# Performance work log

Measured on AMD Instinct MI355X. Metric: run time of the kernel, lower is better.

## Reference

```python
import jax, jax.numpy as jnp
import numpy as np

VOCAB = 50000; EMBED = 300; KDIM = 128; KNUM = 21; KSIZES = (1, 2, 3)
B = 32; QLEN = 32; DLEN = 1024


def _kernel_mus(n):
    mus = [1.0]
    bs = 2.0 / (n - 1)
    mus.append(1.0 - bs / 2)
    for i in range(1, n - 1):
        mus.append(mus[i] - bs)
    return np.asarray(mus, np.float32)


def _kernel_sigmas(n):
    return np.asarray([0.001] + [0.1] * (n - 1), np.float32)


def setup_inputs() -> dict:
    key = jax.random.key(0)
    ks = jax.random.split(key, 12)
    inp = {
        'query_ids': jax.random.randint(ks[0], (B, QLEN), 0, VOCAB),
        'query_masks': jnp.ones((B, QLEN), jnp.float32),
        'doc_ids': jax.random.randint(ks[1], (B, DLEN), 0, VOCAB),
        'doc_masks': jnp.ones((B, DLEN), jnp.float32),
        'emb': jax.random.normal(ks[2], (VOCAB, EMBED), jnp.float32) * 0.02,
    }
    for i, k in enumerate(KSIZES):
        inp[f'conv_w{i+1}'] = jax.random.normal(ks[3 + i], (KDIM, EMBED, k), jnp.float32) / np.sqrt(EMBED * k)
        inp[f'conv_b{i+1}'] = jnp.zeros((KDIM,), jnp.float32)
    feat = KNUM * len(KSIZES) ** 2  # 189
    inp['dense_w'] = jax.random.normal(ks[9], (feat, 1), jnp.float32) * 0.05
    inp['dense_b'] = jnp.zeros((1,), jnp.float32)
    return inp


def _conv_relu(x, w, b):
    # x: [B, L, E], w: [O, E, K] -> [B, L-K+1, O] (VALID conv, matches torch Conv1d no padding)
    y = jax.lax.conv_general_dilated(x, w, (1,), 'VALID', dimension_numbers=('NWC', 'OIW', 'NWC'))
    return jax.nn.relu(y + b)


def _matcher(k_enc, k_mask, v_enc, v_mask, mus, sig):
    kn = k_enc / (jnp.linalg.norm(k_enc, axis=-1, keepdims=True) + 1e-13)
    vn = v_enc / (jnp.linalg.norm(v_enc, axis=-1, keepdims=True) + 1e-13)
    inter = jnp.einsum('bqd,bvd->bqv', kn, vn) * (k_mask[:, :, None] * v_mask[:, None, :])
    # multi-Gaussian soft-histogram over similarity: [B, q, v, KNUM]
    ko = jnp.exp(-((inter[..., None] - mus) ** 2) / (2.0 * sig ** 2))
    kde = jnp.log(jnp.maximum(ko.sum(axis=2), 1e-10)) * 0.01  # [B, q, KNUM]
    return (kde * k_mask[..., None]).sum(axis=1)  # [B, KNUM]


def reference(query_ids, query_masks, doc_ids, doc_masks, emb,
              conv_w1, conv_b1, conv_w2, conv_b2, conv_w3, conv_b3,
              dense_w, dense_b):
    mus = jnp.asarray(_kernel_mus(KNUM))
    sig = jnp.asarray(_kernel_sigmas(KNUM))
    qe = emb[query_ids]  # [B, QLEN, E]
    de = emb[doc_ids]    # [B, DLEN, E]
    cw = [(conv_w1, conv_b1), (conv_w2, conv_b2), (conv_w3, conv_b3)]
    q_encs = [_conv_relu(qe, w, b) for w, b in cw]
    d_encs = [_conv_relu(de, w, b) for w, b in cw]
    logits = jnp.concatenate([
        _matcher(q, query_masks[:, :q.shape[1]], d, doc_masks[:, :d.shape[1]], mus, sig)
        for q in q_encs for d in d_encs], axis=1)  # [B, 189]
    score = (logits @ dense_w + dense_b).squeeze(-1)  # [B]
    return score, logits
```

## Files before the change

kernel.cpp:

```cpp
#include <hip/hip_runtime.h>
#include <hip/hip_bf16.h>
#include <math.h>

#define NB 32
#define QL 32
#define DL 1024
#define EMB 300
#define EMBP 320
#define OD 128
#define KNUM 21
#define VOCAB 50000

typedef short short8 __attribute__((ext_vector_type(8)));
typedef float floatx4 __attribute__((ext_vector_type(4)));

static const size_t WP_OFF  = 0;
static const size_t DPK_OFF = 122880;
static const size_t QPK_OFF = 5365760;
static const size_t QH_OFF  = 5529920;
static const size_t QLO_OFF = 5726528;
static const size_t DH_OFF  = 5923136;
static const size_t DLO_OFF = 12214592;
static const size_t ACC_OFF = 18506048;
static const int ACC_SZ = 9 * NB * QL * KNUM;

#define QPLANE 131072
#define DPLANE 4194304

#define MROWS (NB * DL + NB * QL)
#define MTILES 264
#define CONV_BLOCKS (MTILES * 3)

__device__ __constant__ int WPOFF_C[3] = {0, 40960, 122880};

__device__ __forceinline__ void gl_lds16(const ushort* g, char* l) {
    __builtin_amdgcn_global_load_lds(
        (const __attribute__((address_space(1))) unsigned int*)(g),
        (__attribute__((address_space(3))) unsigned int*)(l), 16, 0, 0);
}

__device__ __forceinline__ ushort bf16_bits(float f) {
    __hip_bfloat16 h = __float2bfloat16(f);
    return *reinterpret_cast<ushort*>(&h);
}

__global__ void prep_w_kernel(const float* __restrict__ w1,
                              const float* __restrict__ w2,
                              const float* __restrict__ w3,
                              ushort* __restrict__ wp) {
    int idx = blockIdx.x * 256 + threadIdx.x;
    if (idx >= 245760) return;
    const float* src;
    int k, rel, base;
    if (idx < 40960)        { k = 1; rel = idx;          src = w1; base = 0; }
    else if (idx < 122880)  { k = 2; rel = idx - 40960;  src = w2; base = 40960; }
    else                    { k = 3; rel = idx - 122880; src = w3; base = 122880; }
    int kd = 320 * k;
    int o = rel / kd;
    int jc = rel - o * kd;
    int j = jc / EMBP;
    int c = jc - j * EMBP;
    float f = (c < EMB) ? src[(o * EMB + c) * k + j] : 0.f;
    wp[base + rel] = bf16_bits(f);
}

__global__ void gather_pack(const float* __restrict__ emb,
                            const int* __restrict__ dids, const int* __restrict__ qids,
                            ushort* __restrict__ dpk, ushort* __restrict__ qpk) {
    int idx = blockIdx.x * 256 + threadIdx.x;
    const int DROWS = NB * DL;
    if (idx >= (DROWS + NB * QL + 2) * 40) return;
    int r = idx / 40;
    int c0 = (idx - r * 40) * 8;
    int rid;
    ushort* dst;
    if (r < DROWS) { rid = dids[r]; dst = dpk + (size_t)r * EMBP; }
    else if (r < DROWS + NB * QL) { rid = qids[r - DROWS]; dst = qpk + (size_t)(r - DROWS) * EMBP; }
    else {
        uint4 zz = {0u, 0u, 0u, 0u};
        *reinterpret_cast<uint4*>(qpk + (size_t)(r - DROWS) * EMBP + c0) = zz;
        return;
    }
    const float* erow = emb + (size_t)rid * EMB;
    ushort v[8];
    if (c0 + 8 <= EMB) {
        float4 f0 = *reinterpret_cast<const float4*>(erow + c0);
        float4 f1 = *reinterpret_cast<const float4*>(erow + c0 + 4);
        float fv[8] = {f0.x, f0.y, f0.z, f0.w, f1.x, f1.y, f1.z, f1.w};
#pragma unroll
        for (int i = 0; i < 8; ++i) v[i] = bf16_bits(fv[i]);
    } else {
#pragma unroll
        for (int i = 0; i < 8; ++i) {
            int c = c0 + i;
            v[i] = bf16_bits((c < EMB) ? erow[c] : 0.f);
        }
    }
    *reinterpret_cast<uint4*>(dst + c0) = *reinterpret_cast<uint4*>(v);
}

__global__ __launch_bounds__(256) void conv_mfma(const ushort* __restrict__ xpk,
                                                 const float* __restrict__ dmask,
                                                 const float* __restrict__ qmask,
                                                 const ushort* __restrict__ wp,
                                                 const float* __restrict__ b1,
                                                 const float* __restrict__ b2,
                                                 const float* __restrict__ b3,
                                                 ushort* __restrict__ dh,
                                                 ushort* __restrict__ dlo,
                                                 ushort* __restrict__ qh,
                                                 ushort* __restrict__ qlo) {
    __shared__ __align__(16) char smem[2][33024];

    const int tid = threadIdx.x;
    const int bid = blockIdx.x;
    const int swz = (bid & 7) * (CONV_BLOCKS / 8) + (bid >> 3);
    const int z = swz % 3;
    const int tile = swz / 3;
    const int l0 = tile * 128;

    const int Kdim = EMBP * (z + 1);
    const int nk = 5 * (z + 1);
    const ushort* wpk = wp + WPOFF_C[z];
    const float* bias = (z == 0) ? b1 : ((z == 1) ? b2 : b3);

    const int wave = tid >> 6;
    const int lane = tid & 63;
    const int l15 = lane & 15;
    const int quad = lane >> 4;
    const int wm = wave >> 1;
    const int wn = wave & 1;

    const int srow = lane >> 3;
    const int scol = (lane & 7) * 8;
    const ushort* a0 = xpk + (size_t)(l0 + wave * 8 + srow) * EMBP + scol;
    const ushort* at = xpk + (size_t)(l0 + 128 + srow) * EMBP + scol;
    const ushort* b0 = wpk + (size_t)(wave * 8 + srow) * Kdim + scol;

    auto stage = [&](int buf, int kk) {
        int jj = (kk >= 10) ? 2 : ((kk >= 5) ? 1 : 0);
        int coff = (kk - jj * 5) * 64;
        int koff = kk * 64;
        char* abuf = smem[buf];
        char* bbuf = smem[buf] + 16640;
#pragma unroll
        for (int p = 0; p < 4; ++p)
            gl_lds16(a0 + p * (32 * EMBP) + coff, abuf + p * 4096 + wave * 1024);
        if (wave == 0 && lane < 16)
            gl_lds16(at + coff, abuf + 16384);
#pragma unroll
        for (int p = 0; p < 4; ++p)
            gl_lds16(b0 + (size_t)p * 32 * Kdim + koff, bbuf + p * 4096 + wave * 1024);
    };

    floatx4 acc[4][4];
#pragma unroll
    for (int i = 0; i < 4; ++i)
#pragma unroll
        for (int j = 0; j < 4; ++j) acc[i][j] = (floatx4)0.f;

    stage(0, 0);
    __syncthreads();

    int jjc = 0, ccc = 0;
    int buf = 0;
    for (int kk = 0; kk < nk; ++kk) {
        if (kk + 1 < nk) stage(buf ^ 1, kk + 1);
        const char* Ab = smem[buf];
        const char* Bb = smem[buf] + 16640;
        short8 af[2][4], bf[2][4];
#pragma unroll
        for (int h = 0; h < 2; ++h)
#pragma unroll
            for (int i = 0; i < 4; ++i) {
                af[h][i] = *reinterpret_cast<const short8*>(
                    Ab + (wm * 64 + i * 16 + l15 + jjc) * 128 + h * 64 + quad * 16);
                bf[h][i] = *reinterpret_cast<const short8*>(
                    Bb + (wn * 64 + i * 16 + l15) * 128 + h * 64 + quad * 16);
            }
#pragma unroll
        for (int h = 0; h < 2; ++h)
#pragma unroll
            for (int i = 0; i < 4; ++i)
#pragma unroll
                for (int j = 0; j < 4; ++j)
                    acc[i][j] = __builtin_amdgcn_mfma_f32_16x16x32_bf16(af[h][i], bf[h][j], acc[i][j], 0, 0, 0);
        ++ccc;
        if (ccc == 5) { ccc = 0; ++jjc; }
        __syncthreads();
        buf ^= 1;
    }

    float (*rowsum)[128] = reinterpret_cast<float(*)[128]>(smem);
    float bv[4];
#pragma unroll
    for (int j = 0; j < 4; ++j) bv[j] = bias[wn * 64 + j * 16 + l15];
#pragma unroll
    for (int i = 0; i < 4; ++i)
#pragma unroll
        for (int r = 0; r < 4; ++r) {
            float p = 0.f;
#pragma unroll
            for (int j = 0; j < 4; ++j) {
                float y = fmaxf(acc[i][j][r] + bv[j], 0.f);
                acc[i][j][r] = y;
                p += y * y;
            }
#pragma unroll
            for (int m = 1; m < 16; m <<= 1) p += __shfl_xor(p, m, 64);
            if (l15 == 0) rowsum[wn][wm * 64 + i * 16 + quad * 4 + r] = p;
        }
    __syncthreads();

#pragma unroll
    for (int i = 0; i < 4; ++i) {
#pragma unroll
        for (int rr = 0; rr < 4; ++rr) {
            int rl = wm * 64 + i * 16 + quad * 4 + rr;
            int r = l0 + rl;
            float tot = rowsum[0][rl] + rowsum[1][rl];
            float mv;
            ushort* hp;
            ushort* lp;
            if (r < NB * DL) {
                int l = r & (DL - 1);
                if (l >= DL - z) continue;
                mv = dmask[r];
                size_t base = (size_t)z * DPLANE + (size_t)r * OD;
                hp = dh + base; lp = dlo + base;
            } else {
                int t = r - NB * DL;
                int l = t & (QL - 1);
                if (l >= QL - z) continue;
                mv = qmask[t];
                size_t base = (size_t)z * QPLANE + (size_t)t * OD;
                hp = qh + base; lp = qlo + base;
            }
            float sc = mv / (sqrtf(tot) + 1e-13f);
            int cb = wn * 64 + l15;
#pragma unroll
            for (int j = 0; j < 4; ++j) {
                float v = acc[i][j][rr] * sc;
                __hip_bfloat16 h = __float2bfloat16(v);
                float hf = __bfloat162float(h);
                hp[cb + j * 16] = *reinterpret_cast<ushort*>(&h);
                __hip_bfloat16 l = __float2bfloat16(v - hf);
                lp[cb + j * 16] = *reinterpret_cast<ushort*>(&l);
            }
        }
    }
}

__global__ __launch_bounds__(256, 4) void matcher_kernel(const ushort* __restrict__ qh_g,
                                                         const ushort* __restrict__ ql_g,
                                                         const ushort* __restrict__ vh_g,
                                                         const ushort* __restrict__ vl_g,
                                                         float* __restrict__ accb) {
    __shared__ __align__(16) float Sm[32 * 132];
    __shared__ float stageb[672];

    const int tid = threadIdx.x;
    const int pp = blockIdx.z;
    const int b = blockIdx.y;
    const int v0 = blockIdx.x * 128;
    const int qi = pp / 3;
    const int di = pp - qi * 3;
    const int Vk = 1024 - di;

    const ushort* qhb = qh_g + (size_t)qi * QPLANE + (size_t)b * (QL * OD);
    const ushort* qlb = ql_g + (size_t)qi * QPLANE + (size_t)b * (QL * OD);
    const ushort* vhb = vh_g + (size_t)di * DPLANE + (size_t)b * (DL * OD) + (size_t)v0 * OD;
    const ushort* vlb = vl_g + (size_t)di * DPLANE + (size_t)b * (DL * OD) + (size_t)v0 * OD;

    const int wave = tid >> 6;
    const int lane = tid & 63;
    const int l15 = lane & 15;
    const int quad = lane >> 4;

    floatx4 acc[2][2];
#pragma unroll
    for (int i = 0; i < 2; ++i)
#pragma unroll
        for (int j = 0; j < 2; ++j) acc[i][j] = (floatx4)0.f;

#pragma unroll
    for (int kw = 0; kw < 4; ++kw) {
        const int ko = kw * 32 + quad * 8;
        short8 qh[2], ql[2], vh[2], vl[2];
#pragma unroll
        for (int i = 0; i < 2; ++i) {
            const int qr = i * 16 + l15;
            const int vr = wave * 32 + i * 16 + l15;
            qh[i] = *reinterpret_cast<const short8*>(qhb + qr * OD + ko);
            ql[i] = *reinterpret_cast<const short8*>(qlb + qr * OD + ko);
            vh[i] = *reinterpret_cast<const short8*>(vhb + (size_t)vr * OD + ko);
            vl[i] = *reinterpret_cast<const short8*>(vlb + (size_t)vr * OD + ko);
        }
#pragma unroll
        for (int i = 0; i < 2; ++i)
#pragma unroll
            for (int j = 0; j < 2; ++j) {
                acc[i][j] = __builtin_amdgcn_mfma_f32_16x16x32_bf16(qh[i], vh[j], acc[i][j], 0, 0, 0);
                acc[i][j] = __builtin_amdgcn_mfma_f32_16x16x32_bf16(qh[i], vl[j], acc[i][j], 0, 0, 0);
                acc[i][j] = __builtin_amdgcn_mfma_f32_16x16x32_bf16(ql[i], vh[j], acc[i][j], 0, 0, 0);
            }
    }

    const int vmax = min(128, Vk - v0);
#pragma unroll
    for (int i = 0; i < 2; ++i)
#pragma unroll
        for (int j = 0; j < 2; ++j)
#pragma unroll
            for (int r = 0; r < 4; ++r) {
                int q = i * 16 + quad * 4 + r;
                int v = wave * 32 + j * 16 + l15;
                float val = acc[i][j][r];
                if (v >= vmax) val = 1.0e4f;
                Sm[q * 132 + v] = val;
            }
    __syncthreads();

    {
        const int q = tid >> 3;
        const int c = tid & 7;
        const float* srow = &Sm[q * 132 + c * 16];
        const float Am  = -72.13475204f;
        const float Am5 = -14.426950408f;
        const float A0  = -721347.52f;
        const float C   = 0x1.0p-126f;

        float s00 = 0.f, s01 = 0.f, s02 = 0.f, s03 = 0.f, s04 = 0.f, s05 = 0.f,
              s06 = 0.f, s07 = 0.f, s08 = 0.f, s09 = 0.f, s10 = 0.f, s11 = 0.f,
              s12 = 0.f, s13 = 0.f, s14 = 0.f, s15 = 0.f, s16 = 0.f, s17 = 0.f,
              s18 = 0.f, s19 = 0.f, s20 = 0.f;

#define GACC(B) { B = __builtin_fmaf(tx, C, B); B = __builtin_fmaf(ty, C, B); \
                  B = __builtin_fmaf(tz, C, B); B = __builtin_fmaf(tw, C, B); }
#define GSTEP(B, g) { tx *= Rx * (g); ty *= Ry * (g); tz *= Rz * (g); tw *= Rw * (g); GACC(B) }

#pragma unroll
        for (int jj = 0; jj < 4; ++jj) {
            float4 s4 = *reinterpret_cast<const float4*>(srow + jj * 4);
            float dx = s4.x - 0.95f, dy = s4.y - 0.95f, dz = s4.z - 0.95f, dwv = s4.w - 0.95f;
            float tx = __builtin_exp2f(__builtin_fmaf(Am * dx, dx, 126.f));
            float ty = __builtin_exp2f(__builtin_fmaf(Am * dy, dy, 126.f));
            float tz = __builtin_exp2f(__builtin_fmaf(Am * dz, dz, 126.f));
            float tw = __builtin_exp2f(__builtin_fmaf(Am * dwv, dwv, 126.f));
            float Rx = __builtin_exp2f(Am5 * dx);
            float Ry = __builtin_exp2f(Am5 * dy);
            float Rz = __builtin_exp2f(Am5 * dz);
            float Rw = __builtin_exp2f(Am5 * dwv);
            GACC(s01)
            GSTEP(s02, 6.0653066e-01f) GSTEP(s03, 2.2313016e-01f)
            GSTEP(s04, 8.2084999e-02f) GSTEP(s05, 3.0197383e-02f)
            GSTEP(s06, 1.1108997e-02f) GSTEP(s07, 4.0867714e-03f)
            GSTEP(s08, 1.5034391e-03f) GSTEP(s09, 5.5308438e-04f)
            GSTEP(s10, 2.0346837e-04f) GSTEP(s11, 7.4851830e-05f)
            GSTEP(s12, 2.7536450e-05f) GSTEP(s13, 1.0130095e-05f)
            GSTEP(s14, 3.7266532e-06f) GSTEP(s15, 1.3709590e-06f)
            GSTEP(s16, 5.0434766e-07f) GSTEP(s17, 1.8553914e-07f)
            GSTEP(s18, 6.8256033e-08f) GSTEP(s19, 2.5110699e-08f)
            GSTEP(s20, 9.2374496e-09f)
            float ex = s4.x - 1.f, ey = s4.y - 1.f, ez = s4.z - 1.f, ew = s4.w - 1.f;
            s00 += __builtin_exp2f((A0 * ex) * ex);
            s00 += __builtin_exp2f((A0 * ey) * ey);
            s00 += __builtin_exp2f((A0 * ez) * ez);
            s00 += __builtin_exp2f((A0 * ew) * ew);
        }
#undef GSTEP
#undef GACC

#define GRED(B) { B += __shfl_xor(B, 1, 64); B += __shfl_xor(B, 2, 64); B += __shfl_xor(B, 4, 64); }
        GRED(s00) GRED(s01) GRED(s02) GRED(s03) GRED(s04) GRED(s05) GRED(s06)
        GRED(s07) GRED(s08) GRED(s09) GRED(s10) GRED(s11) GRED(s12) GRED(s13)
        GRED(s14) GRED(s15) GRED(s16) GRED(s17) GRED(s18) GRED(s19) GRED(s20)
#undef GRED
        if (c == 0) {
            float* sp = &stageb[q * KNUM];
            sp[0]  = s00; sp[1]  = s01; sp[2]  = s02; sp[3]  = s03; sp[4]  = s04;
            sp[5]  = s05; sp[6]  = s06; sp[7]  = s07; sp[8]  = s08; sp[9]  = s09;
            sp[10] = s10; sp[11] = s11; sp[12] = s12; sp[13] = s13; sp[14] = s14;
            sp[15] = s15; sp[16] = s16; sp[17] = s17; sp[18] = s18; sp[19] = s19;
            sp[20] = s20;
        }
    }
    __syncthreads();

    {
        float* dst = &accb[((size_t)(pp * NB + b) * QL) * KNUM];
        for (int i = tid; i < 32 * KNUM; i += 256)
            atomicAdd(dst + i, stageb[i]);
    }
}

__global__ void finalize_kernel(const float* __restrict__ accb,
                                const float* __restrict__ qmask,
                                const float* __restrict__ dw,
                                const float* __restrict__ db,
                                float* __restrict__ out) {
    __shared__ float prod[192];
    int b = blockIdx.x;
    int tid = threadIdx.x;
    if (tid < 189) {
        int pq = tid / 21;
        int t = tid - pq * 21;
        int qi = pq / 3;
        int Qk = 32 - qi;
        const float* ab = accb + ((pq * NB + b) * QL) * KNUM + t;
        float s = 0.f;
        for (int q = 0; q < Qk; ++q)
            s += logf(fmaxf(ab[q * KNUM], 1e-10f)) * qmask[b * QL + q];
        float lg = s * 0.01f;
        out[NB + b * 189 + tid] = lg;
        prod[tid] = lg * dw[tid];
    }
    __syncthreads();
    if (tid == 0) {
        float sc = db[0];
        for (int i = 0; i < 189; ++i) sc += prod[i];
        out[b] = sc;
    }
}

extern "C" void kernel_launch(void* const* d_in, const int* in_sizes, int n_in,
                              void* d_out, int out_size, void* d_ws, size_t ws_size,
                              hipStream_t stream) {
    const int* qids = (const int*)d_in[0];
    const float* qmask = (const float*)d_in[1];
    const int* dids = (const int*)d_in[2];
    const float* dmask = (const float*)d_in[3];
    const float* emb = (const float*)d_in[4];
    const float* w1 = (const float*)d_in[5];
    const float* b1 = (const float*)d_in[6];
    const float* w2 = (const float*)d_in[7];
    const float* b2 = (const float*)d_in[8];
    const float* w3 = (const float*)d_in[9];
    const float* b3 = (const float*)d_in[10];
    const float* dw = (const float*)d_in[11];
    const float* db = (const float*)d_in[12];
    float* out = (float*)d_out;
    float* ws = (float*)d_ws;

    ushort* wp  = (ushort*)(ws + WP_OFF);
    ushort* dpk = (ushort*)(ws + DPK_OFF);
    ushort* qpk = (ushort*)(ws + QPK_OFF);
    ushort* qh  = (ushort*)(ws + QH_OFF);
    ushort* qlo = (ushort*)(ws + QLO_OFF);
    ushort* dh  = (ushort*)(ws + DH_OFF);
    ushort* dlo = (ushort*)(ws + DLO_OFF);
    float* accb = ws + ACC_OFF;

    hipMemsetAsync(accb, 0, ACC_SZ * sizeof(float), stream);
    prep_w_kernel<<<960, 256, 0, stream>>>(w1, w2, w3, wp);
    gather_pack<<<((MROWS + 2) * 40 + 255) / 256, 256, 0, stream>>>(emb, dids, qids, dpk, qpk);

    conv_mfma<<<CONV_BLOCKS, 256, 0, stream>>>(dpk, dmask, qmask, wp, b1, b2, b3, dh, dlo, qh, qlo);

    matcher_kernel<<<dim3(8, NB, 9), 256, 0, stream>>>(qh, qlo, dh, dlo, accb);
    finalize_kernel<<<NB, 256, 0, stream>>>(accb, qmask, dw, db, out);
}
```

Baseline: 228.7 us.

## Merge weight prep with gather and XOR-swizzle conv LDS tiles

Folds the weight-packing kernel and the embedding gather kernel into one launch by splitting the index range, which removes one kernel launch and its serialization gap. In the conv MFMA kernel, each lane now loads the global column chunk chosen by XORing its chunk index with its row index modulo 8, and the LDS fragment reads apply the same XOR, so tiles land in LDS in swizzled order. This is meant to cut LDS bank conflicts on the 128-byte-row fragment reads. The swizzle must match exactly between the global-to-LDS loads and the reads, and the shifted A-row offset (jjc) makes that mapping easy to get wrong.

```diff
diff --git a/kernel.cpp b/kernel.cpp
--- a/kernel.cpp
+++ b/kernel.cpp
@@ -31,6 +31,9 @@
 #define MTILES 264
 #define CONV_BLOCKS (MTILES * 3)
 
+#define PREPW_N 245760
+#define GATHER_N ((MROWS + 2) * 40)
+
 __device__ __constant__ int WPOFF_C[3] = {0, 40960, 122880};
 
 __device__ __forceinline__ void gl_lds16(const ushort* g, char* l) {
@@ -44,32 +47,31 @@
     return *reinterpret_cast<ushort*>(&h);
 }
 
-__global__ void prep_w_kernel(const float* __restrict__ w1,
-                              const float* __restrict__ w2,
-                              const float* __restrict__ w3,
-                              ushort* __restrict__ wp) {
+__global__ void gather_prep(const float* __restrict__ emb,
+                            const int* __restrict__ dids, const int* __restrict__ qids,
+                            const float* __restrict__ w1, const float* __restrict__ w2,
+                            const float* __restrict__ w3,
+                            ushort* __restrict__ dpk, ushort* __restrict__ qpk,
+                            ushort* __restrict__ wp) {
     int idx = blockIdx.x * 256 + threadIdx.x;
-    if (idx >= 245760) return;
-    const float* src;
-    int k, rel, base;
-    if (idx < 40960)        { k = 1; rel = idx;          src = w1; base = 0; }
-    else if (idx < 122880)  { k = 2; rel = idx - 40960;  src = w2; base = 40960; }
-    else                    { k = 3; rel = idx - 122880; src = w3; base = 122880; }
-    int kd = 320 * k;
-    int o = rel / kd;
-    int jc = rel - o * kd;
-    int j = jc / EMBP;
-    int c = jc - j * EMBP;
-    float f = (c < EMB) ? src[(o * EMB + c) * k + j] : 0.f;
-    wp[base + rel] = bf16_bits(f);
-}
-
-__global__ void gather_pack(const float* __restrict__ emb,
-                            const int* __restrict__ dids, const int* __restrict__ qids,
-                            ushort* __restrict__ dpk, ushort* __restrict__ qpk) {
-    int idx = blockIdx.x * 256 + threadIdx.x;
+    if (idx < PREPW_N) {
+        const float* src;
+        int k, rel, base;
+        if (idx < 40960)        { k = 1; rel = idx;          src = w1; base = 0; }
+        else if (idx < 122880)  { k = 2; rel = idx - 40960;  src = w2; base = 40960; }
+        else                    { k = 3; rel = idx - 122880; src = w3; base = 122880; }
+        int kd = 320 * k;
+        int o = rel / kd;
+        int jc = rel - o * kd;
+        int j = jc / EMBP;
+        int c = jc - j * EMBP;
+        float f = (c < EMB) ? src[(o * EMB + c) * k + j] : 0.f;
+        wp[base + rel] = bf16_bits(f);
+        return;
+    }
+    idx -= PREPW_N;
+    if (idx >= GATHER_N) return;
     const int DROWS = NB * DL;
-    if (idx >= (DROWS + NB * QL + 2) * 40) return;
     int r = idx / 40;
     int c0 = (idx - r * 40) * 8;
     int rid;
@@ -132,10 +134,10 @@
     const int wn = wave & 1;
 
     const int srow = lane >> 3;
-    const int scol = (lane & 7) * 8;
-    const ushort* a0 = xpk + (size_t)(l0 + wave * 8 + srow) * EMBP + scol;
-    const ushort* at = xpk + (size_t)(l0 + 128 + srow) * EMBP + scol;
-    const ushort* b0 = wpk + (size_t)(wave * 8 + srow) * Kdim + scol;
+    const int scolx = (((lane & 7) ^ (lane >> 3) ^ 0) & 7) * 8;
+    const ushort* a0 = xpk + (size_t)(l0 + wave * 8 + srow) * EMBP + scolx;
+    const ushort* at = xpk + (size_t)(l0 + 128 + srow) * EMBP + scolx;
+    const ushort* b0 = wpk + (size_t)(wave * 8 + srow) * Kdim + scolx;
 
     auto stage = [&](int buf, int kk) {
         int jj = (kk >= 10) ? 2 : ((kk >= 5) ? 1 : 0);
@@ -173,10 +175,12 @@
         for (int h = 0; h < 2; ++h)
 #pragma unroll
             for (int i = 0; i < 4; ++i) {
+                int ra = wm * 64 + i * 16 + l15 + jjc;
+                int rb = wn * 64 + i * 16 + l15;
                 af[h][i] = *reinterpret_cast<const short8*>(
-                    Ab + (wm * 64 + i * 16 + l15 + jjc) * 128 + h * 64 + quad * 16);
+                    Ab + ra * 128 + ((((h << 2) | quad) ^ (ra & 7)) << 4));
                 bf[h][i] = *reinterpret_cast<const short8*>(
-                    Bb + (wn * 64 + i * 16 + l15) * 128 + h * 64 + quad * 16);
+                    Bb + rb * 128 + ((((h << 2) | quad) ^ (rb & 7)) << 4));
             }
 #pragma unroll
         for (int h = 0; h < 2; ++h)
@@ -452,8 +456,8 @@
     float* accb = ws + ACC_OFF;
 
     hipMemsetAsync(accb, 0, ACC_SZ * sizeof(float), stream);
-    prep_w_kernel<<<960, 256, 0, stream>>>(w1, w2, w3, wp);
-    gather_pack<<<((MROWS + 2) * 40 + 255) / 256, 256, 0, stream>>>(emb, dids, qids, dpk, qpk);
+    gather_prep<<<(PREPW_N + GATHER_N + 255) / 256, 256, 0, stream>>>(
+        emb, dids, qids, w1, w2, w3, dpk, qpk, wp);
 
     conv_mfma<<<CONV_BLOCKS, 256, 0, stream>>>(dpk, dmask, qmask, wp, b1, b2, b3, dh, dlo, qh, qlo);
 
```

After: 220.4 us. 1.04x faster.
